# Performance work log

Measured on AMD Instinct MI355X. Metric: run time of the kernel, lower is better.

Reference implementation:

```python
import jax, jax.numpy as jnp
import numpy as np

B, T, D, H = 4, 2048, 1024, 64

def setup_inputs() -> dict:
    key = jax.random.key(0)
    kx, kq, kk, kv = jax.random.split(key, 4)
    s = 1.0 / np.sqrt(D)
    return {
        "x": jax.random.normal(kx, (B, T, D), dtype=jnp.float32),
        "Wq": jax.random.normal(kq, (D, H), dtype=jnp.float32) * s,
        "Wk": jax.random.normal(kk, (D, H), dtype=jnp.float32) * s,
        "Wv": jax.random.normal(kv, (D, H), dtype=jnp.float32) * s,
    }

def reference(x, Wq, Wk, Wv):
    # q,k,v: [B,T,H]
    q = jnp.einsum('btd,dh->bth', x, Wq)
    k = jnp.einsum('btd,dh->bth', x, Wk)
    v = jnp.einsum('btd,dh->bth', x, Wv)
    scale = jnp.asarray(H, x.dtype) ** -0.5
    wei = jnp.einsum('bqh,bkh->bqk', q, k) * scale  # [B,T,T]
    Tlen = x.shape[1]
    causal = jnp.tril(jnp.ones((Tlen, Tlen), dtype=bool))
    wei = jnp.where(causal, wei, -jnp.inf)
    attn = jax.nn.softmax(wei, axis=-1)
    return jnp.einsum('bqk,bkh->bqh', attn, v)
```

## Files before the change

kernel.cpp:

```cpp
#include <hip/hip_runtime.h>
#include <hip/hip_bf16.h>
#include <math.h>

#define Bb   4
#define Tlen 2048
#define Dd   1024
#define Hh   64
#define NROWS 8192
#define NQ   32
#define NC   4

typedef short bf16x8 __attribute__((ext_vector_type(8)));
typedef float f32x4  __attribute__((ext_vector_type(4)));

__device__ __forceinline__ unsigned short f2b(float f) {
    unsigned u = __float_as_uint(f);
    unsigned r = u + 0x7FFFu + ((u >> 16) & 1u);
    return (unsigned short)(r >> 16);
}
__device__ __forceinline__ unsigned pk2(float a, float b) {
    __hip_bfloat162 h = __float22bfloat162_rn(make_float2(a, b));
    return *reinterpret_cast<unsigned*>(&h);
}

__global__ __launch_bounds__(256) void wtrans_kernel(
    const float* __restrict__ Wq, const float* __restrict__ Wk,
    const float* __restrict__ Wv, unsigned short* __restrict__ wfrag)
{
    const int s = blockIdx.x * 256 + threadIdx.x;
    const int f   = s / 768;
    const int rem = s % 768;
    const int nb  = rem >> 6;
    const int lane = rem & 63;
    const int g = lane >> 4, qr = lane & 15;
    const int n = nb * 16 + qr;
    const int wsel = n >> 6, h = n & 63;
    const float* W = (wsel == 0) ? Wq : (wsel == 1) ? Wk : Wv;
    const int k0 = (f >> 1) * 64 + (f & 1) * 32 + g * 8;
    unsigned short tmp[8];
    #pragma unroll
    for (int j = 0; j < 8; ++j) tmp[j] = f2b(W[(size_t)(k0 + j) * Hh + h]);
    *(bf16x8*)(wfrag + (size_t)s * 8) = *(const bf16x8*)tmp;
}

__global__ __launch_bounds__(256) void proj_kernel(
    const float* __restrict__ x, const unsigned short* __restrict__ wfrag,
    unsigned short* __restrict__ qw, unsigned short* __restrict__ kw,
    unsigned short* __restrict__ vw)
{
    __shared__ unsigned short xs[2][32 * 64];

    const int rb   = blockIdx.x * 32;
    const int tid  = threadIdx.x;
    const int wv   = tid >> 6;
    const int lane = tid & 63;
    const int qr   = lane & 15;
    const int g    = lane >> 4;

    const int xr = tid >> 3, xc8 = tid & 7;
    const float* xg0 = x + (size_t)(rb + xr) * Dd + xc8 * 8;

    const unsigned short* wp = wfrag + ((size_t)(wv * 3) * 64 + lane) * 8;

    f32x4 acc[6] = {};

    float4 px0 = *(const float4*)(xg0 + 0);
    float4 px1 = *(const float4*)(xg0 + 4);

    #pragma unroll
    for (int t = 0; t < 16; ++t) {
        const int cur = t & 1;
        {
            union { unsigned u[4]; bf16x8 v; } p8;
            p8.u[0] = pk2(px0.x, px0.y);
            p8.u[1] = pk2(px0.z, px0.w);
            p8.u[2] = pk2(px1.x, px1.y);
            p8.u[3] = pk2(px1.z, px1.w);
            *(bf16x8*)(&xs[cur][xr * 64 + ((xc8 ^ (xr & 7)) << 3)]) = p8.v;
        }
        __syncthreads();

        if (t < 15) {
            px0 = *(const float4*)(xg0 + (t + 1) * 64 + 0);
            px1 = *(const float4*)(xg0 + (t + 1) * 64 + 4);
        }

        #pragma unroll
        for (int ks = 0; ks < 2; ++ks) {
            const int f = t * 2 + ks;
            bf16x8 b0 = *(const bf16x8*)(wp + (size_t)(f * 12 + 0) * 512);
            bf16x8 b1 = *(const bf16x8*)(wp + (size_t)(f * 12 + 1) * 512);
            bf16x8 b2 = *(const bf16x8*)(wp + (size_t)(f * 12 + 2) * 512);
            #pragma unroll
            for (int mf = 0; mf < 2; ++mf) {
                const int arow = mf * 16 + qr;
                const bf16x8 a = *(const bf16x8*)(
                    &xs[cur][arow * 64 + (((ks * 4 + g) ^ (arow & 7)) << 3)]);
                acc[mf * 3 + 0] = __builtin_amdgcn_mfma_f32_16x16x32_bf16(a, b0, acc[mf * 3 + 0], 0, 0, 0);
                acc[mf * 3 + 1] = __builtin_amdgcn_mfma_f32_16x16x32_bf16(a, b1, acc[mf * 3 + 1], 0, 0, 0);
                acc[mf * 3 + 2] = __builtin_amdgcn_mfma_f32_16x16x32_bf16(a, b2, acc[mf * 3 + 2], 0, 0, 0);
            }
        }
        __syncthreads();
    }

    #pragma unroll
    for (int mf = 0; mf < 2; ++mf) {
        #pragma unroll
        for (int nf = 0; nf < 3; ++nf) {
            const int n = wv * 48 + nf * 16 + qr;
            const int wsel = n >> 6, h = n & 63;
            unsigned short* out = (wsel == 0) ? qw : (wsel == 1) ? kw : vw;
            const f32x4 ov = acc[mf * 3 + nf];
            #pragma unroll
            for (int r = 0; r < 4; ++r)
                out[(size_t)(rb + mf * 16 + 4 * g + r) * Hh + h] = f2b(ov[r]);
        }
    }
}

#define XSTR 72
#define VSTR 40
__global__ __launch_bounds__(256) void attn_kernel(
    const unsigned short* __restrict__ qw, const unsigned short* __restrict__ kw,
    const unsigned short* __restrict__ vw,
    float* __restrict__ part_O, float* __restrict__ part_ml)
{
    __shared__ unsigned short ks_s[32 * XSTR];
    __shared__ unsigned short vt_s[64 * VSTR];

    const int qt = (NQ - 1) - blockIdx.x;
    const int ci = blockIdx.y;
    const int b  = blockIdx.z;
    const int tid = threadIdx.x;
    const int wv = tid >> 6, lane = tid & 63;
    const int qr = lane & 15, g = lane >> 4;

    const int ntk = 2 * qt + 2;
    const int tpc = (ntk + NC - 1) / NC;
    const int t0  = ci * tpc;
    const int t1  = (ntk < t0 + tpc) ? ntk : (t0 + tpc);

    const size_t base = (size_t)b * Tlen * Hh;
    const int qrow = qt * 64 + wv * 16 + qr;

    const bf16x8 qf0 = *(const bf16x8*)(qw + base + (size_t)qrow * Hh + 8 * g);
    const bf16x8 qf1 = *(const bf16x8*)(qw + base + (size_t)qrow * Hh + 32 + 8 * g);

    f32x4 o0 = {}, o1 = {}, o2 = {}, o3 = {};
    float m = -INFINITY, l = 0.f;

    for (int kt = t0; kt < t1; ++kt) {
        const int j0 = kt * 32;
        __syncthreads();
        {
            const int row = tid >> 3, cg = tid & 7;
            const bf16x8 k8 = *(const bf16x8*)(kw + base + (size_t)(j0 + row) * Hh + cg * 8);
            *(bf16x8*)(&ks_s[row * XSTR + ((cg ^ (row & 3)) << 3)]) = k8;
            const bf16x8 v8 = *(const bf16x8*)(vw + base + (size_t)(j0 + row) * Hh + cg * 8);
            #pragma unroll
            for (int u = 0; u < 8; ++u) {
                const int c = cg * 8 + u;
                const int jx = row ^ (((c >> 3) & 3) << 3);
                vt_s[c * VSTR + jx] = ((const unsigned short*)&v8)[u];
            }
        }
        __syncthreads();

        f32x4 a0 = {}, a1 = {};
        {
            const int sw = (g ^ (qr & 3)) << 3;
            bf16x8 kf;
            kf = *(const bf16x8*)(&ks_s[qr * XSTR + sw]);
            a0 = __builtin_amdgcn_mfma_f32_16x16x32_bf16(kf, qf0, a0, 0, 0, 0);
            kf = *(const bf16x8*)(&ks_s[qr * XSTR + 32 + sw]);
            a0 = __builtin_amdgcn_mfma_f32_16x16x32_bf16(kf, qf1, a0, 0, 0, 0);
            kf = *(const bf16x8*)(&ks_s[(16 + qr) * XSTR + sw]);
            a1 = __builtin_amdgcn_mfma_f32_16x16x32_bf16(kf, qf0, a1, 0, 0, 0);
            kf = *(const bf16x8*)(&ks_s[(16 + qr) * XSTR + 32 + sw]);
            a1 = __builtin_amdgcn_mfma_f32_16x16x32_bf16(kf, qf1, a1, 0, 0, 0);
        }

        float p[8];
        float tm = -INFINITY;
        #pragma unroll
        for (int jf = 0; jf < 2; ++jf) {
            #pragma unroll
            for (int r = 0; r < 4; ++r) {
                const int jg = j0 + jf * 16 + 4 * g + r;
                float s = ((jf == 0) ? a0[r] : a1[r]) * 0.125f;
                s = (jg > qrow) ? -INFINITY : s;
                p[jf * 4 + r] = s;
                tm = fmaxf(tm, s);
            }
        }
        tm = fmaxf(tm, __shfl_xor(tm, 16));
        tm = fmaxf(tm, __shfl_xor(tm, 32));
        const float mnew  = fmaxf(m, tm);
        const float alpha = (m == -INFINITY) ? 0.f : __expf(m - mnew);
        float psum = 0.f;
        #pragma unroll
        for (int i = 0; i < 8; ++i) {
            const float pv = (p[i] == -INFINITY) ? 0.f : __expf(p[i] - mnew);
            p[i] = pv; psum += pv;
        }
        psum += __shfl_xor(psum, 16);
        psum += __shfl_xor(psum, 32);
        l = l * alpha + psum;
        m = mnew;

        const float ar0 = __shfl(alpha, 4 * g + 0);
        const float ar1 = __shfl(alpha, 4 * g + 1);
        const float ar2 = __shfl(alpha, 4 * g + 2);
        const float ar3 = __shfl(alpha, 4 * g + 3);
        o0[0] *= ar0; o0[1] *= ar1; o0[2] *= ar2; o0[3] *= ar3;
        o1[0] *= ar0; o1[1] *= ar1; o1[2] *= ar2; o1[3] *= ar3;
        o2[0] *= ar0; o2[1] *= ar1; o2[2] *= ar2; o2[3] *= ar3;
        o3[0] *= ar0; o3[1] *= ar1; o3[2] *= ar2; o3[3] *= ar3;

        unsigned pw[4];
        pw[0] = f2b(p[0]) | ((unsigned)f2b(p[1]) << 16);
        pw[1] = f2b(p[2]) | ((unsigned)f2b(p[3]) << 16);
        pw[2] = f2b(p[4]) | ((unsigned)f2b(p[5]) << 16);
        pw[3] = f2b(p[6]) | ((unsigned)f2b(p[7]) << 16);
        union PU { unsigned u[4]; bf16x8 v; } pu;
        #pragma unroll
        for (int w = 0; w < 4; ++w) {
            const int gp  = 2 * g + (w >> 1);
            const int src = 16 * (gp & 3) + qr;
            const unsigned t0s = __shfl(pw[0 + (w & 1)], src);
            const unsigned t1s = __shfl(pw[2 + (w & 1)], src);
            pu.u[w] = (gp & 4) ? t1s : t0s;
        }
        const bf16x8 pa = pu.v;

        {
            int cb = qr;
            bf16x8 vf = *(const bf16x8*)(&vt_s[cb * VSTR + 8 * (g ^ ((cb >> 3) & 3))]);
            o0 = __builtin_amdgcn_mfma_f32_16x16x32_bf16(pa, vf, o0, 0, 0, 0);
            cb = 16 + qr;
            vf = *(const bf16x8*)(&vt_s[cb * VSTR + 8 * (g ^ ((cb >> 3) & 3))]);
            o1 = __builtin_amdgcn_mfma_f32_16x16x32_bf16(pa, vf, o1, 0, 0, 0);
            cb = 32 + qr;
            vf = *(const bf16x8*)(&vt_s[cb * VSTR + 8 * (g ^ ((cb >> 3) & 3))]);
            o2 = __builtin_amdgcn_mfma_f32_16x16x32_bf16(pa, vf, o2, 0, 0, 0);
            cb = 48 + qr;
            vf = *(const bf16x8*)(&vt_s[cb * VSTR + 8 * (g ^ ((cb >> 3) & 3))]);
            o3 = __builtin_amdgcn_mfma_f32_16x16x32_bf16(pa, vf, o3, 0, 0, 0);
        }
    }

    const int blin = (b * NQ + qt) * NC + ci;
    float* po = part_O + (size_t)blin * 4096;
    #pragma unroll
    for (int nf = 0; nf < 4; ++nf) {
        const f32x4 ov = (nf == 0) ? o0 : (nf == 1) ? o1 : (nf == 2) ? o2 : o3;
        #pragma unroll
        for (int r = 0; r < 4; ++r)
            po[(size_t)(wv * 16 + 4 * g + r) * 64 + nf * 16 + qr] = ov[r];
    }
    if (g == 0) {
        part_ml[(size_t)blin * 128 + wv * 16 + qr]      = m;
        part_ml[(size_t)blin * 128 + 64 + wv * 16 + qr] = l;
    }
}

__global__ __launch_bounds__(256) void merge_kernel(
    const float* __restrict__ part_O, const float* __restrict__ part_ml,
    float* __restrict__ out)
{
    const int idx = blockIdx.x * 256 + threadIdx.x;
    const int row = idx >> 6;
    const int c   = idx & 63;
    const int b   = row >> 11;
    const int t   = row & 2047;
    const int qt  = t >> 6;
    const int qq  = t & 63;
    const int bl0 = (b * NQ + qt) * NC;

    float M = -INFINITY;
    #pragma unroll
    for (int i = 0; i < NC; ++i) {
        const float lvi = part_ml[(size_t)(bl0 + i) * 128 + 64 + qq];
        if (lvi > 0.f) M = fmaxf(M, part_ml[(size_t)(bl0 + i) * 128 + qq]);
    }
    float num = 0.f, den = 0.f;
    #pragma unroll
    for (int i = 0; i < NC; ++i) {
        const float lvi = part_ml[(size_t)(bl0 + i) * 128 + 64 + qq];
        if (lvi > 0.f) {
            const float wgt = __expf(part_ml[(size_t)(bl0 + i) * 128 + qq] - M);
            num += wgt * part_O[(size_t)(bl0 + i) * 4096 + (size_t)qq * 64 + c];
            den += wgt * lvi;
        }
    }
    out[(size_t)row * 64 + c] = num / den;
}

extern "C" void kernel_launch(void* const* d_in, const int* in_sizes, int n_in,
                              void* d_out, int out_size, void* d_ws, size_t ws_size,
                              hipStream_t stream) {
    const float* x  = (const float*)d_in[0];
    const float* Wq = (const float*)d_in[1];
    const float* Wk = (const float*)d_in[2];
    const float* Wv = (const float*)d_in[3];
    float* outp = (float*)d_out;

    unsigned short* wfrag = (unsigned short*)d_ws;
    unsigned short* qw = wfrag + 192 * 1024;
    unsigned short* kw = qw + NROWS * Hh;
    unsigned short* vw = kw + NROWS * Hh;
    float* part_O  = (float*)(vw + NROWS * Hh);
    float* part_ml = part_O + (size_t)(Bb * NQ * NC) * 4096;

    wtrans_kernel<<<dim3(96), 256, 0, stream>>>(Wq, Wk, Wv, wfrag);
    proj_kernel<<<dim3(NROWS / 32), 256, 0, stream>>>(x, wfrag, qw, kw, vw);
    attn_kernel<<<dim3(NQ, NC, Bb), 256, 0, stream>>>(qw, kw, vw, part_O, part_ml);
    merge_kernel<<<dim3((NROWS * Hh) / 256), 256, 0, stream>>>(part_O, part_ml, outp);
}
```

Measured before the change: 49.34 us.

## Use 64-key tiles, register prefetch, and adaptive split-K chunking in attention

The attention kernel now processes 64 keys per iteration instead of 32, so each LDS barrier pair and online-softmax rescale covers twice as many MFMAs. K/V for the next tile are loaded into registers while the current tile computes. The split across blocks is now adaptive: up to 8 chunks per query tile, sized to its causal length, with idle blocks exiting early. The merge kernel loops over the actual chunk count. The cost is more register and LDS pressure, a larger partial-output workspace, and a changed V-transpose swizzle.

Result: slower. 54.00 us (+9.4%).

```diff
diff --git a/kernel.cpp b/kernel.cpp
--- a/kernel.cpp
+++ b/kernel.cpp
@@ -8,7 +8,7 @@
 #define Hh   64
 #define NROWS 8192
 #define NQ   32
-#define NC   4
+#define MAXCH 8
 
 typedef short bf16x8 __attribute__((ext_vector_type(8)));
 typedef float f32x4  __attribute__((ext_vector_type(4)));
@@ -119,76 +119,95 @@
     }
 }
 
-#define XSTR 72
-#define VSTR 40
+#define KXSTR 72
+#define VTSTR 72
 __global__ __launch_bounds__(256) void attn_kernel(
     const unsigned short* __restrict__ qw, const unsigned short* __restrict__ kw,
     const unsigned short* __restrict__ vw,
     float* __restrict__ part_O, float* __restrict__ part_ml)
 {
-    __shared__ unsigned short ks_s[32 * XSTR];
-    __shared__ unsigned short vt_s[64 * VSTR];
+    __shared__ unsigned short ks_s[64 * KXSTR];
+    __shared__ unsigned short vt_s[64 * VTSTR];
 
     const int qt = (NQ - 1) - blockIdx.x;
     const int ci = blockIdx.y;
     const int b  = blockIdx.z;
+
+    const int ntk = qt + 1;
+    const int nch = min(MAXCH, (ntk + 1) >> 1);
+    const int C   = (ntk + nch - 1) / nch;
+    const int nuse = (ntk + C - 1) / C;
+    if (ci >= nuse) return;
+    const int t0 = ci * C;
+    const int t1 = (ntk < t0 + C) ? ntk : (t0 + C);
+
     const int tid = threadIdx.x;
     const int wv = tid >> 6, lane = tid & 63;
     const int qr = lane & 15, g = lane >> 4;
 
-    const int ntk = 2 * qt + 2;
-    const int tpc = (ntk + NC - 1) / NC;
-    const int t0  = ci * tpc;
-    const int t1  = (ntk < t0 + tpc) ? ntk : (t0 + tpc);
-
     const size_t base = (size_t)b * Tlen * Hh;
     const int qrow = qt * 64 + wv * 16 + qr;
 
     const bf16x8 qf0 = *(const bf16x8*)(qw + base + (size_t)qrow * Hh + 8 * g);
     const bf16x8 qf1 = *(const bf16x8*)(qw + base + (size_t)qrow * Hh + 32 + 8 * g);
 
-    f32x4 o0 = {}, o1 = {}, o2 = {}, o3 = {};
+    f32x4 o[4] = {};
     float m = -INFINITY, l = 0.f;
 
+    const int row_a = tid >> 3, cg_a = tid & 7;
+    const int row_b = 32 + row_a, cg_b = cg_a;
+    const unsigned short* kA = kw + base + (size_t)row_a * Hh + cg_a * 8;
+    const unsigned short* kB = kw + base + (size_t)row_b * Hh + cg_b * 8;
+    const unsigned short* vA = vw + base + (size_t)row_a * Hh + cg_a * 8;
+    const unsigned short* vB = vw + base + (size_t)row_b * Hh + cg_b * 8;
+
+    bf16x8 k8a, k8b, v8a, v8b;
+    {
+        const size_t off = (size_t)t0 * 64 * Hh;
+        k8a = *(const bf16x8*)(kA + off);  k8b = *(const bf16x8*)(kB + off);
+        v8a = *(const bf16x8*)(vA + off);  v8b = *(const bf16x8*)(vB + off);
+    }
+
     for (int kt = t0; kt < t1; ++kt) {
-        const int j0 = kt * 32;
+        const int j0 = kt * 64;
         __syncthreads();
-        {
-            const int row = tid >> 3, cg = tid & 7;
-            const bf16x8 k8 = *(const bf16x8*)(kw + base + (size_t)(j0 + row) * Hh + cg * 8);
-            *(bf16x8*)(&ks_s[row * XSTR + ((cg ^ (row & 3)) << 3)]) = k8;
-            const bf16x8 v8 = *(const bf16x8*)(vw + base + (size_t)(j0 + row) * Hh + cg * 8);
-            #pragma unroll
-            for (int u = 0; u < 8; ++u) {
-                const int c = cg * 8 + u;
-                const int jx = row ^ (((c >> 3) & 3) << 3);
-                vt_s[c * VSTR + jx] = ((const unsigned short*)&v8)[u];
-            }
+        *(bf16x8*)(&ks_s[row_a * KXSTR + ((cg_a ^ (row_a & 3)) << 3)]) = k8a;
+        *(bf16x8*)(&ks_s[row_b * KXSTR + ((cg_b ^ (row_b & 3)) << 3)]) = k8b;
+        #pragma unroll
+        for (int u = 0; u < 8; ++u) {
+            const int ca = cg_a * 8 + u;
+            vt_s[ca * VTSTR + (((row_a >> 3) ^ (ca & 7)) << 3) + (row_a & 7)] =
+                ((const unsigned short*)&v8a)[u];
+            vt_s[ca * VTSTR + (((row_b >> 3) ^ (ca & 7)) << 3) + (row_b & 7)] =
+                ((const unsigned short*)&v8b)[u];
         }
         __syncthreads();
 
-        f32x4 a0 = {}, a1 = {};
-        {
-            const int sw = (g ^ (qr & 3)) << 3;
-            bf16x8 kf;
-            kf = *(const bf16x8*)(&ks_s[qr * XSTR + sw]);
-            a0 = __builtin_amdgcn_mfma_f32_16x16x32_bf16(kf, qf0, a0, 0, 0, 0);
-            kf = *(const bf16x8*)(&ks_s[qr * XSTR + 32 + sw]);
-            a0 = __builtin_amdgcn_mfma_f32_16x16x32_bf16(kf, qf1, a0, 0, 0, 0);
-            kf = *(const bf16x8*)(&ks_s[(16 + qr) * XSTR + sw]);
-            a1 = __builtin_amdgcn_mfma_f32_16x16x32_bf16(kf, qf0, a1, 0, 0, 0);
-            kf = *(const bf16x8*)(&ks_s[(16 + qr) * XSTR + 32 + sw]);
-            a1 = __builtin_amdgcn_mfma_f32_16x16x32_bf16(kf, qf1, a1, 0, 0, 0);
-        }
-
-        float p[8];
+        if (kt + 1 < t1) {
+            const size_t off = (size_t)(kt + 1) * 64 * Hh;
+            k8a = *(const bf16x8*)(kA + off);  k8b = *(const bf16x8*)(kB + off);
+            v8a = *(const bf16x8*)(vA + off);  v8b = *(const bf16x8*)(vB + off);
+        }
+
+        f32x4 a[4] = {};
+        #pragma unroll
+        for (int jf = 0; jf < 4; ++jf) {
+            const int row = jf * 16 + qr;
+            const int sw = ((g ^ (row & 3)) << 3);
+            bf16x8 kf = *(const bf16x8*)(&ks_s[row * KXSTR + sw]);
+            a[jf] = __builtin_amdgcn_mfma_f32_16x16x32_bf16(kf, qf0, a[jf], 0, 0, 0);
+            kf = *(const bf16x8*)(&ks_s[row * KXSTR + 32 + sw]);
+            a[jf] = __builtin_amdgcn_mfma_f32_16x16x32_bf16(kf, qf1, a[jf], 0, 0, 0);
+        }
+
+        float p[16];
         float tm = -INFINITY;
         #pragma unroll
-        for (int jf = 0; jf < 2; ++jf) {
+        for (int jf = 0; jf < 4; ++jf) {
             #pragma unroll
             for (int r = 0; r < 4; ++r) {
                 const int jg = j0 + jf * 16 + 4 * g + r;
-                float s = ((jf == 0) ? a0[r] : a1[r]) * 0.125f;
+                float s = a[jf][r] * 0.125f;
                 s = (jg > qrow) ? -INFINITY : s;
                 p[jf * 4 + r] = s;
                 tm = fmaxf(tm, s);
@@ -200,7 +219,7 @@
         const float alpha = (m == -INFINITY) ? 0.f : __expf(m - mnew);
         float psum = 0.f;
         #pragma unroll
-        for (int i = 0; i < 8; ++i) {
+        for (int i = 0; i < 16; ++i) {
             const float pv = (p[i] == -INFINITY) ? 0.f : __expf(p[i] - mnew);
             p[i] = pv; psum += pv;
         }
@@ -213,51 +232,47 @@
         const float ar1 = __shfl(alpha, 4 * g + 1);
         const float ar2 = __shfl(alpha, 4 * g + 2);
         const float ar3 = __shfl(alpha, 4 * g + 3);
-        o0[0] *= ar0; o0[1] *= ar1; o0[2] *= ar2; o0[3] *= ar3;
-        o1[0] *= ar0; o1[1] *= ar1; o1[2] *= ar2; o1[3] *= ar3;
-        o2[0] *= ar0; o2[1] *= ar1; o2[2] *= ar2; o2[3] *= ar3;
-        o3[0] *= ar0; o3[1] *= ar1; o3[2] *= ar2; o3[3] *= ar3;
-
-        unsigned pw[4];
-        pw[0] = f2b(p[0]) | ((unsigned)f2b(p[1]) << 16);
-        pw[1] = f2b(p[2]) | ((unsigned)f2b(p[3]) << 16);
-        pw[2] = f2b(p[4]) | ((unsigned)f2b(p[5]) << 16);
-        pw[3] = f2b(p[6]) | ((unsigned)f2b(p[7]) << 16);
-        union PU { unsigned u[4]; bf16x8 v; } pu;
+        #pragma unroll
+        for (int nf = 0; nf < 4; ++nf) {
+            o[nf][0] *= ar0; o[nf][1] *= ar1; o[nf][2] *= ar2; o[nf][3] *= ar3;
+        }
+
+        unsigned pw[8];
+        #pragma unroll
+        for (int jf = 0; jf < 4; ++jf) {
+            pw[jf * 2 + 0] = f2b(p[jf * 4 + 0]) | ((unsigned)f2b(p[jf * 4 + 1]) << 16);
+            pw[jf * 2 + 1] = f2b(p[jf * 4 + 2]) | ((unsigned)f2b(p[jf * 4 + 3]) << 16);
+        }
+        union PU { unsigned u[4]; bf16x8 v; } pl, ph;
         #pragma unroll
         for (int w = 0; w < 4; ++w) {
-            const int gp  = 2 * g + (w >> 1);
-            const int src = 16 * (gp & 3) + qr;
-            const unsigned t0s = __shfl(pw[0 + (w & 1)], src);
-            const unsigned t1s = __shfl(pw[2 + (w & 1)], src);
-            pu.u[w] = (gp & 4) ? t1s : t0s;
-        }
-        const bf16x8 pa = pu.v;
-
-        {
-            int cb = qr;
-            bf16x8 vf = *(const bf16x8*)(&vt_s[cb * VSTR + 8 * (g ^ ((cb >> 3) & 3))]);
-            o0 = __builtin_amdgcn_mfma_f32_16x16x32_bf16(pa, vf, o0, 0, 0, 0);
-            cb = 16 + qr;
-            vf = *(const bf16x8*)(&vt_s[cb * VSTR + 8 * (g ^ ((cb >> 3) & 3))]);
-            o1 = __builtin_amdgcn_mfma_f32_16x16x32_bf16(pa, vf, o1, 0, 0, 0);
-            cb = 32 + qr;
-            vf = *(const bf16x8*)(&vt_s[cb * VSTR + 8 * (g ^ ((cb >> 3) & 3))]);
-            o2 = __builtin_amdgcn_mfma_f32_16x16x32_bf16(pa, vf, o2, 0, 0, 0);
-            cb = 48 + qr;
-            vf = *(const bf16x8*)(&vt_s[cb * VSTR + 8 * (g ^ ((cb >> 3) & 3))]);
-            o3 = __builtin_amdgcn_mfma_f32_16x16x32_bf16(pa, vf, o3, 0, 0, 0);
-        }
-    }
-
-    const int blin = (b * NQ + qt) * NC + ci;
+            const int src = 16 * ((g & 1) * 2 + (w >> 1)) + qr;
+            const unsigned s0 = __shfl(pw[0 + (w & 1)], src);
+            const unsigned s1 = __shfl(pw[2 + (w & 1)], src);
+            const unsigned s2 = __shfl(pw[4 + (w & 1)], src);
+            const unsigned s3 = __shfl(pw[6 + (w & 1)], src);
+            pl.u[w] = (g >> 1) ? s1 : s0;
+            ph.u[w] = (g >> 1) ? s3 : s2;
+        }
+        const bf16x8 pa0 = pl.v, pa1 = ph.v;
+
+        #pragma unroll
+        for (int nf = 0; nf < 4; ++nf) {
+            const int c = nf * 16 + qr;
+            bf16x8 vf = *(const bf16x8*)(&vt_s[c * VTSTR + (((0 + g) ^ (c & 7)) << 3)]);
+            o[nf] = __builtin_amdgcn_mfma_f32_16x16x32_bf16(pa0, vf, o[nf], 0, 0, 0);
+            vf = *(const bf16x8*)(&vt_s[c * VTSTR + (((4 + g) ^ (c & 7)) << 3)]);
+            o[nf] = __builtin_amdgcn_mfma_f32_16x16x32_bf16(pa1, vf, o[nf], 0, 0, 0);
+        }
+    }
+
+    const int blin = (b * NQ + qt) * MAXCH + ci;
     float* po = part_O + (size_t)blin * 4096;
     #pragma unroll
     for (int nf = 0; nf < 4; ++nf) {
-        const f32x4 ov = (nf == 0) ? o0 : (nf == 1) ? o1 : (nf == 2) ? o2 : o3;
         #pragma unroll
         for (int r = 0; r < 4; ++r)
-            po[(size_t)(wv * 16 + 4 * g + r) * 64 + nf * 16 + qr] = ov[r];
+            po[(size_t)(wv * 16 + 4 * g + r) * 64 + nf * 16 + qr] = o[nf][r];
     }
     if (g == 0) {
         part_ml[(size_t)blin * 128 + wv * 16 + qr]      = m;
@@ -276,23 +291,22 @@
     const int t   = row & 2047;
     const int qt  = t >> 6;
     const int qq  = t & 63;
-    const int bl0 = (b * NQ + qt) * NC;
+
+    const int ntk = qt + 1;
+    const int nch = min(MAXCH, (ntk + 1) >> 1);
+    const int C   = (ntk + nch - 1) / nch;
+    const int nuse = (ntk + C - 1) / C;
+    const int bl0 = (b * NQ + qt) * MAXCH;
 
     float M = -INFINITY;
-    #pragma unroll
-    for (int i = 0; i < NC; ++i) {
+    for (int i = 0; i < nuse; ++i)
+        M = fmaxf(M, part_ml[(size_t)(bl0 + i) * 128 + qq]);
+    float num = 0.f, den = 0.f;
+    for (int i = 0; i < nuse; ++i) {
         const float lvi = part_ml[(size_t)(bl0 + i) * 128 + 64 + qq];
-        if (lvi > 0.f) M = fmaxf(M, part_ml[(size_t)(bl0 + i) * 128 + qq]);
-    }
-    float num = 0.f, den = 0.f;
-    #pragma unroll
-    for (int i = 0; i < NC; ++i) {
-        const float lvi = part_ml[(size_t)(bl0 + i) * 128 + 64 + qq];
-        if (lvi > 0.f) {
-            const float wgt = __expf(part_ml[(size_t)(bl0 + i) * 128 + qq] - M);
-            num += wgt * part_O[(size_t)(bl0 + i) * 4096 + (size_t)qq * 64 + c];
-            den += wgt * lvi;
-        }
+        const float wgt = __expf(part_ml[(size_t)(bl0 + i) * 128 + qq] - M);
+        num += wgt * part_O[(size_t)(bl0 + i) * 4096 + (size_t)qq * 64 + c];
+        den += wgt * lvi;
     }
     out[(size_t)row * 64 + c] = num / den;
 }
@@ -311,10 +325,10 @@
     unsigned short* kw = qw + NROWS * Hh;
     unsigned short* vw = kw + NROWS * Hh;
     float* part_O  = (float*)(vw + NROWS * Hh);
-    float* part_ml = part_O + (size_t)(Bb * NQ * NC) * 4096;
+    float* part_ml = part_O + (size_t)(Bb * NQ * MAXCH) * 4096;
 
     wtrans_kernel<<<dim3(96), 256, 0, stream>>>(Wq, Wk, Wv, wfrag);
     proj_kernel<<<dim3(NROWS / 32), 256, 0, stream>>>(x, wfrag, qw, kw, vw);
-    attn_kernel<<<dim3(NQ, NC, Bb), 256, 0, stream>>>(qw, kw, vw, part_O, part_ml);
+    attn_kernel<<<dim3(NQ, MAXCH, Bb), 256, 0, stream>>>(qw, kw, vw, part_O, part_ml);
     merge_kernel<<<dim3((NROWS * Hh) / 256), 256, 0, stream>>>(part_O, part_ml, outp);
 }
```

## Prefetch weights and K/V tiles into registers; skip rescale when max unchanged

Applied to the files above, without the earlier changes.

The projection kernel now loads the next step's weight fragments into registers one iteration early instead of loading them right before the MFMAs. The attention kernel prefetches the next K/V tile from global memory into registers while the current tile is being computed. The online-softmax rescale is skipped when no row max grows in the wave, and the -inf checks are replaced by clamping the max. This hides global-load latency and trims ALU work, at the cost of more registers and a possible drop in occupancy.

New measurement: 48.52 us. Within noise of the previous version (-1.7%).

```diff
diff --git a/kernel.cpp b/kernel.cpp
--- a/kernel.cpp
+++ b/kernel.cpp
@@ -67,6 +67,13 @@
     float4 px0 = *(const float4*)(xg0 + 0);
     float4 px1 = *(const float4*)(xg0 + 4);
 
+    bf16x8 wr[6];
+    #pragma unroll
+    for (int ks = 0; ks < 2; ++ks)
+        #pragma unroll
+        for (int nf = 0; nf < 3; ++nf)
+            wr[ks * 3 + nf] = *(const bf16x8*)(wp + (size_t)(ks * 12 + nf) * 512);
+
     #pragma unroll
     for (int t = 0; t < 16; ++t) {
         const int cur = t & 1;
@@ -80,28 +87,36 @@
         }
         __syncthreads();
 
+        bf16x8 wn[6];
         if (t < 15) {
             px0 = *(const float4*)(xg0 + (t + 1) * 64 + 0);
             px1 = *(const float4*)(xg0 + (t + 1) * 64 + 4);
+            const int fb = (t + 1) * 2;
+            #pragma unroll
+            for (int ks = 0; ks < 2; ++ks)
+                #pragma unroll
+                for (int nf = 0; nf < 3; ++nf)
+                    wn[ks * 3 + nf] = *(const bf16x8*)(wp + (size_t)((fb + ks) * 12 + nf) * 512);
         }
 
         #pragma unroll
         for (int ks = 0; ks < 2; ++ks) {
-            const int f = t * 2 + ks;
-            bf16x8 b0 = *(const bf16x8*)(wp + (size_t)(f * 12 + 0) * 512);
-            bf16x8 b1 = *(const bf16x8*)(wp + (size_t)(f * 12 + 1) * 512);
-            bf16x8 b2 = *(const bf16x8*)(wp + (size_t)(f * 12 + 2) * 512);
             #pragma unroll
             for (int mf = 0; mf < 2; ++mf) {
                 const int arow = mf * 16 + qr;
                 const bf16x8 a = *(const bf16x8*)(
                     &xs[cur][arow * 64 + (((ks * 4 + g) ^ (arow & 7)) << 3)]);
-                acc[mf * 3 + 0] = __builtin_amdgcn_mfma_f32_16x16x32_bf16(a, b0, acc[mf * 3 + 0], 0, 0, 0);
-                acc[mf * 3 + 1] = __builtin_amdgcn_mfma_f32_16x16x32_bf16(a, b1, acc[mf * 3 + 1], 0, 0, 0);
-                acc[mf * 3 + 2] = __builtin_amdgcn_mfma_f32_16x16x32_bf16(a, b2, acc[mf * 3 + 2], 0, 0, 0);
+                acc[mf * 3 + 0] = __builtin_amdgcn_mfma_f32_16x16x32_bf16(a, wr[ks * 3 + 0], acc[mf * 3 + 0], 0, 0, 0);
+                acc[mf * 3 + 1] = __builtin_amdgcn_mfma_f32_16x16x32_bf16(a, wr[ks * 3 + 1], acc[mf * 3 + 1], 0, 0, 0);
+                acc[mf * 3 + 2] = __builtin_amdgcn_mfma_f32_16x16x32_bf16(a, wr[ks * 3 + 2], acc[mf * 3 + 2], 0, 0, 0);
             }
         }
         __syncthreads();
+
+        if (t < 15) {
+            #pragma unroll
+            for (int i = 0; i < 6; ++i) wr[i] = wn[i];
+        }
     }
 
     #pragma unroll
@@ -150,22 +165,34 @@
     f32x4 o0 = {}, o1 = {}, o2 = {}, o3 = {};
     float m = -INFINITY, l = 0.f;
 
+    const int srow = tid >> 3, scg = tid & 7;
+    const unsigned short* kbase = kw + base + (size_t)srow * Hh + scg * 8;
+    const unsigned short* vbase = vw + base + (size_t)srow * Hh + scg * 8;
+    const int ksw = ((scg ^ (srow & 3)) << 3);
+    bf16x8 k8 = {}, v8 = {};
+    if (t0 < t1) {
+        k8 = *(const bf16x8*)(kbase + (size_t)t0 * 32 * Hh);
+        v8 = *(const bf16x8*)(vbase + (size_t)t0 * 32 * Hh);
+    }
+
     for (int kt = t0; kt < t1; ++kt) {
         const int j0 = kt * 32;
         __syncthreads();
         {
-            const int row = tid >> 3, cg = tid & 7;
-            const bf16x8 k8 = *(const bf16x8*)(kw + base + (size_t)(j0 + row) * Hh + cg * 8);
-            *(bf16x8*)(&ks_s[row * XSTR + ((cg ^ (row & 3)) << 3)]) = k8;
-            const bf16x8 v8 = *(const bf16x8*)(vw + base + (size_t)(j0 + row) * Hh + cg * 8);
+            *(bf16x8*)(&ks_s[srow * XSTR + ksw]) = k8;
             #pragma unroll
             for (int u = 0; u < 8; ++u) {
-                const int c = cg * 8 + u;
-                const int jx = row ^ (((c >> 3) & 3) << 3);
+                const int c = scg * 8 + u;
+                const int jx = srow ^ (((c >> 3) & 3) << 3);
                 vt_s[c * VSTR + jx] = ((const unsigned short*)&v8)[u];
             }
         }
         __syncthreads();
+
+        if (kt + 1 < t1) {
+            k8 = *(const bf16x8*)(kbase + (size_t)(kt + 1) * 32 * Hh);
+            v8 = *(const bf16x8*)(vbase + (size_t)(kt + 1) * 32 * Hh);
+        }
 
         f32x4 a0 = {}, a1 = {};
         {
@@ -196,27 +223,32 @@
         }
         tm = fmaxf(tm, __shfl_xor(tm, 16));
         tm = fmaxf(tm, __shfl_xor(tm, 32));
-        const float mnew  = fmaxf(m, tm);
-        const float alpha = (m == -INFINITY) ? 0.f : __expf(m - mnew);
+        const float mnew = fmaxf(m, tm);
+        const float mc   = fmaxf(mnew, -1e30f);
         float psum = 0.f;
         #pragma unroll
         for (int i = 0; i < 8; ++i) {
-            const float pv = (p[i] == -INFINITY) ? 0.f : __expf(p[i] - mnew);
+            const float pv = __expf(p[i] - mc);
             p[i] = pv; psum += pv;
         }
         psum += __shfl_xor(psum, 16);
         psum += __shfl_xor(psum, 32);
-        l = l * alpha + psum;
+
+        if (!__all(tm <= m)) {
+            const float alpha = (m == -INFINITY) ? 0.f : __expf(m - mc);
+            const float ar0 = __shfl(alpha, 4 * g + 0);
+            const float ar1 = __shfl(alpha, 4 * g + 1);
+            const float ar2 = __shfl(alpha, 4 * g + 2);
+            const float ar3 = __shfl(alpha, 4 * g + 3);
+            o0[0] *= ar0; o0[1] *= ar1; o0[2] *= ar2; o0[3] *= ar3;
+            o1[0] *= ar0; o1[1] *= ar1; o1[2] *= ar2; o1[3] *= ar3;
+            o2[0] *= ar0; o2[1] *= ar1; o2[2] *= ar2; o2[3] *= ar3;
+            o3[0] *= ar0; o3[1] *= ar1; o3[2] *= ar2; o3[3] *= ar3;
+            l = l * alpha + psum;
+        } else {
+            l += psum;
+        }
         m = mnew;
-
-        const float ar0 = __shfl(alpha, 4 * g + 0);
-        const float ar1 = __shfl(alpha, 4 * g + 1);
-        const float ar2 = __shfl(alpha, 4 * g + 2);
-        const float ar3 = __shfl(alpha, 4 * g + 3);
-        o0[0] *= ar0; o0[1] *= ar1; o0[2] *= ar2; o0[3] *= ar3;
-        o1[0] *= ar0; o1[1] *= ar1; o1[2] *= ar2; o1[3] *= ar3;
-        o2[0] *= ar0; o2[1] *= ar1; o2[2] *= ar2; o2[3] *= ar3;
-        o3[0] *= ar0; o3[1] *= ar1; o3[2] *= ar2; o3[3] *= ar3;
 
         unsigned pw[4];
         pw[0] = f2b(p[0]) | ((unsigned)f2b(p[1]) << 16);
```
